# Performance work log

Measured on AMD Instinct MI355X. Metric: run time of the kernel, lower is better.

The kernel has to match this reference:

```python
import jax, jax.numpy as jnp
import numpy as np

D_MODEL, D_STATE, D_CONV, EXPAND = 1024, 16, 4, 2
D_INNER = EXPAND * D_MODEL           # 2048
DT_RANK = D_MODEL // 16              # 64
BATCH, SEQLEN = 2, 2048


def setup_inputs() -> dict:
    key = jax.random.key(0)
    ks = jax.random.split(key, 10)
    s = 0.02
    hidden_states = jax.random.normal(ks[0], (BATCH, SEQLEN, D_MODEL), jnp.float32)
    in_proj_w = jax.random.normal(ks[1], (2 * D_INNER, D_MODEL), jnp.float32) * s
    conv_w = jax.random.normal(ks[2], (D_INNER, 1, D_CONV), jnp.float32) * 0.3
    conv_b = jax.random.normal(ks[3], (D_INNER,), jnp.float32) * 0.1
    x_proj_w = jax.random.normal(ks[4], (DT_RANK + 2 * D_STATE, D_INNER), jnp.float32) * s
    dt_init_std = DT_RANK ** -0.5
    dt_proj_w = jax.random.uniform(ks[5], (D_INNER, DT_RANK), jnp.float32,
                                   minval=-dt_init_std, maxval=dt_init_std)
    # bias = inverse-softplus of dt sampled log-uniform in [1e-3, 1e-1]
    dt = jnp.exp(jax.random.uniform(ks[6], (D_INNER,), jnp.float32)
                 * (np.log(0.1) - np.log(0.001)) + np.log(0.001))
    dt = jnp.clip(dt, 1e-4, None)
    dt_proj_b = dt + jnp.log(-jnp.expm1(-dt))
    # A = repeat(arange(1, d_state+1), 'n -> d n')
    A_log = jnp.log(jnp.tile(jnp.arange(1, D_STATE + 1, dtype=jnp.float32), (D_INNER, 1)))
    Dp = jnp.ones((D_INNER,), jnp.float32)
    out_proj_w = jax.random.normal(ks[7], (D_MODEL, D_INNER), jnp.float32) * s
    return {
        'hidden_states': hidden_states, 'in_proj_w': in_proj_w,
        'conv_w': conv_w, 'conv_b': conv_b, 'x_proj_w': x_proj_w,
        'dt_proj_w': dt_proj_w, 'dt_proj_b': dt_proj_b,
        'A_log': A_log, 'D': Dp, 'out_proj_w': out_proj_w,
    }


def _mamba_fwd(hidden_states, in_proj_w, conv_w, conv_b, x_proj_w,
               dt_proj_w, dt_proj_b, A_log, D, out_proj_w):
    d_inner = in_proj_w.shape[0] // 2
    d_conv = conv_w.shape[-1]
    dt_rank = dt_proj_w.shape[1]
    d_state = A_log.shape[1]
    b = hidden_states.shape[0]

    # in_proj then split into x / z gate branches  -> [B, L, d_inner] each
    xz = hidden_states @ in_proj_w.T
    x, z = jnp.split(xz, 2, axis=-1)

    # depthwise causal conv1d + SiLU (pad left d_conv-1 == padding=d_conv-1 then trim)
    xc = x.transpose(0, 2, 1)                       # [B, d_inner, L]
    xc = jax.lax.conv_general_dilated(
        xc, conv_w, window_strides=(1,), padding=[(d_conv - 1, 0)],
        dimension_numbers=('NCH', 'OIH', 'NCH'), feature_group_count=d_inner)
    xl = jax.nn.silu(xc + conv_b[None, :, None]).transpose(0, 2, 1)  # [B, L, d_inner]

    # x_proj -> dt, B, C
    x_dbl = xl @ x_proj_w.T                         # [B, L, dt_rank + 2*d_state]
    dt, Bm, Cm = jnp.split(x_dbl, [dt_rank, dt_rank + d_state], axis=-1)
    delta = jax.nn.softplus(dt @ dt_proj_w.T + dt_proj_b)  # [B, L, d_inner]

    A = -jnp.exp(A_log)                             # [d_inner, d_state]

    def step(h, inputs):
        u_t, d_t, b_t, c_t = inputs  # [B,d_inner], [B,d_inner], [B,d_state], [B,d_state]
        dA = jnp.exp(d_t[..., None] * A)                      # [B, d_inner, d_state]
        h = dA * h + (d_t * u_t)[..., None] * b_t[:, None, :]
        y_t = jnp.einsum('bdn,bn->bd', h, c_t)
        return h, y_t

    h0 = jnp.zeros((b, d_inner, d_state), hidden_states.dtype)
    xs = (xl.transpose(1, 0, 2), delta.transpose(1, 0, 2),
          Bm.transpose(1, 0, 2), Cm.transpose(1, 0, 2))
    _, ys = jax.lax.scan(step, h0, xs)              # ys: [L, B, d_inner]
    y = ys.transpose(1, 0, 2)

    y = y + xl * D                                  # skip (D) term
    y = y * jax.nn.silu(z)                          # gate
    return y @ out_proj_w.T                         # [B, L, d_model]


def reference(hidden_states, in_proj_w, conv_w, conv_b, x_proj_w,
              dt_proj_w, dt_proj_b, A_log, D, out_proj_w):
    return _mamba_fwd(hidden_states, in_proj_w, conv_w, conv_b, x_proj_w,
                      dt_proj_w, dt_proj_b, A_log, D, out_proj_w)
```

## Files before the change

kernel.cpp:

```cpp
#include <hip/hip_runtime.h>

#define D_MODEL 1024
#define D_STATE 16
#define D_CONV  4
#define D_INNER 2048
#define DT_RANK 64
#define BATCH   2
#define SEQLEN  2048
#define NTOK    (BATCH * SEQLEN)
#define NCH     64
#define LC      (SEQLEN / NCH)
#define XKS     8
#define XNC     96


__device__ __forceinline__ float bf2f(unsigned short v) {
    union { unsigned int u; float f; } c; c.u = ((unsigned int)v) << 16; return c.f;
}
__device__ __forceinline__ unsigned short f2bf(float f) {
    union { unsigned int u; float f; } c; c.f = f;
    unsigned int r = c.u + 0x7FFF + ((c.u >> 16) & 1);
    return (unsigned short)(r >> 16);
}

__device__ __forceinline__ int sniff_bf(const void* Dp) {
    return (((const unsigned int*)Dp)[0] == 0x3F803F80u) ? 1 : 0;
}

__device__ __forceinline__ float ldF(const void* p, size_t idx, int isbf) {
    return isbf ? bf2f(((const unsigned short*)p)[idx]) : ((const float*)p)[idx];
}
__device__ __forceinline__ void ld16f(const float* p, float* o) {
#pragma unroll
    for (int q = 0; q < 4; q++) {
        float4 v = *(const float4*)(p + 4 * q);
        o[4 * q + 0] = v.x; o[4 * q + 1] = v.y; o[4 * q + 2] = v.z; o[4 * q + 3] = v.w;
    }
}

#define CVT_N0 (NTOK * D_MODEL)
#define CVT_N1 (2 * D_INNER * D_MODEL)
#define CVT_N2 (D_MODEL * D_INNER)
#define CVT_N3 (D_INNER * DT_RANK)
#define CVT_TOT (CVT_N0 + CVT_N1 + CVT_N2 + CVT_N3)

__device__ __forceinline__ void cvt8(const void* in, unsigned short* out,
                                     size_t e0, int isbf)
{
    if (isbf) {
        *(uint4*)(out + e0) = *(const uint4*)((const unsigned short*)in + e0);
    } else {
        const float* f = (const float*)in + e0;
        float4 a = *(const float4*)f;
        float4 b = *(const float4*)(f + 4);
        ushort4 o0 = { f2bf(a.x), f2bf(a.y), f2bf(a.z), f2bf(a.w) };
        ushort4 o1 = { f2bf(b.x), f2bf(b.y), f2bf(b.z), f2bf(b.w) };
        *(ushort4*)(out + e0)     = o0;
        *(ushort4*)(out + e0 + 4) = o1;
    }
}

__launch_bounds__(256)
__global__ void cvt_all(const void* __restrict__ hid, const void* __restrict__ ipw,
                        const void* __restrict__ opw, const void* __restrict__ dtw,
                        unsigned short* __restrict__ hidB, unsigned short* __restrict__ ipwB,
                        unsigned short* __restrict__ opwB, unsigned short* __restrict__ dtwB,
                        const void* __restrict__ Dp)
{
    const int isbf = sniff_bf(Dp);
    size_t e = ((size_t)blockIdx.x * 256 + threadIdx.x) * 8;
    if (e < CVT_N0) { cvt8(hid, hidB, e, isbf); return; }
    e -= CVT_N0;
    if (e < CVT_N1) { cvt8(ipw, ipwB, e, isbf); return; }
    e -= CVT_N1;
    if (e < CVT_N2) { cvt8(opw, opwB, e, isbf); return; }
    e -= CVT_N2;
    if (e < CVT_N3) { cvt8(dtw, dtwB, e, isbf); }
}

typedef __attribute__((ext_vector_type(8))) __bf16 bf16x8;
typedef __attribute__((ext_vector_type(4))) float  f32x4;

__global__ void mfma_probe(int* __restrict__ dmap) {
    __shared__ alignas(16) unsigned short As[16 * 32];
    __shared__ alignas(16) unsigned short Bs[16 * 32];
    const int t = threadIdx.x;
    const int q = t >> 4, l15 = t & 15;

    for (int idx = t; idx < 512; idx += 64) {
        As[idx] = f2bf((float)(idx >> 5));
        Bs[idx] = f2bf(0.03125f);
    }
    __syncthreads();
    bf16x8 a1 = *(const bf16x8*)&As[l15 * 32 + q * 8];
    bf16x8 b1 = *(const bf16x8*)&Bs[l15 * 32 + q * 8];
    f32x4 acc1 = {0.f, 0.f, 0.f, 0.f};
    acc1 = __builtin_amdgcn_mfma_f32_16x16x32_bf16(a1, b1, acc1, 0, 0, 0);
    __syncthreads();

    for (int idx = t; idx < 512; idx += 64) {
        As[idx] = f2bf(0.03125f);
        Bs[idx] = f2bf((float)(idx >> 5));
    }
    __syncthreads();
    bf16x8 a2 = *(const bf16x8*)&As[l15 * 32 + q * 8];
    bf16x8 b2 = *(const bf16x8*)&Bs[l15 * 32 + q * 8];
    f32x4 acc2 = {0.f, 0.f, 0.f, 0.f};
    acc2 = __builtin_amdgcn_mfma_f32_16x16x32_bf16(a2, b2, acc2, 0, 0, 0);

#pragma unroll
    for (int r = 0; r < 4; r++) {
        int ma = (int)(acc1[r] + 0.5f);
        int nb = (int)(acc2[r] + 0.5f);
        if (ma < 0 || ma > 15 || nb < 0 || nb > 15) { ma = q * 4 + r; nb = l15; }
        dmap[t * 4 + r] = ma | (nb << 4);
    }
}

__device__ __forceinline__ void gl2lds16(const void* g, void* l) {
    __builtin_amdgcn_global_load_lds(
        (const __attribute__((address_space(1))) unsigned int*)g,
        (__attribute__((address_space(3))) unsigned int*)l,
        16, 0, 0);
}

__device__ __forceinline__ void stage_half(const unsigned short* __restrict__ G,
                                           int grow0, int K, int k0,
                                           unsigned short* ldsAB, int half, int t)
{
    const int r8  = t >> 3;
    const int c8  = t & 7;
    const int swz = (c8 ^ (r8 & 7)) << 3;
#pragma unroll
    for (int j = 0; j < 2; j++) {
        const int row = half * 128 + j * 64 + r8;
        gl2lds16(&G[(size_t)(grow0 + row) * K + k0 + swz],
                 &ldsAB[row * 64 + c8 * 8]);
    }
}

__device__ __forceinline__ bf16x8 ldsfrag(const unsigned short* p, int row, int slot) {
    return *(const bf16x8*)&p[row * 64 + ((slot ^ (row & 7)) << 3)];
}

__launch_bounds__(512)
__global__ void gemm1_8ph(const unsigned short* __restrict__ A,
                          const unsigned short* __restrict__ B,
                          float* __restrict__ C,
                          int M, int N, int K,
                          const int* __restrict__ dmap)
{
    extern __shared__ __align__(16) unsigned short lds[];
    unsigned short* A0l = lds;
    unsigned short* B0l = lds + 16384;
    unsigned short* A1l = lds + 32768;
    unsigned short* B1l = lds + 49152;

    const int t    = threadIdx.x;
    const int lane = t & 63;
    const int w    = t >> 6;
    const int wm   = (w >> 2) * 128, wn = (w & 3) * 64;
    const int q    = lane >> 4, l15 = lane & 15;

    const int nbn  = N >> 8;
    const int nwg  = (M >> 8) * nbn;
    const int orig = blockIdx.x;
    const int wg   = (orig & 7) * (nwg >> 3) + (orig >> 3);
    const int bm   = wg / nbn, bn = wg % nbn;
    const int m0   = bm << 8, n0 = bn << 8;
    const int NT   = K >> 6;

    int mp[4];
#pragma unroll
    for (int r = 0; r < 4; r++) mp[r] = dmap[lane * 4 + r];

    f32x4 acc[8][4];
#pragma unroll
    for (int i = 0; i < 8; i++)
#pragma unroll
        for (int j = 0; j < 4; j++) acc[i][j] = (f32x4){0.f, 0.f, 0.f, 0.f};

    stage_half(B, n0, K, 0, B0l, 0, t);
    stage_half(B, n0, K, 0, B0l, 1, t);
    stage_half(A, m0, K, 0, A0l, 0, t);
    stage_half(A, m0, K, 0, A0l, 1, t);
    {
        const int k1 = (NT > 1 ? 64 : 0);
        stage_half(B, n0, K, k1, B1l, 0, t);
        stage_half(B, n0, K, k1, B1l, 1, t);
    }
    asm volatile("s_waitcnt vmcnt(4)" ::: "memory");
    __builtin_amdgcn_s_barrier();

#pragma unroll 2
    for (int tt = 0; tt < NT; ++tt) {
        const int p = tt & 1;
        const unsigned short* Ac = p ? A1l : A0l;
        const unsigned short* Bc = p ? B1l : B0l;
        unsigned short* Anx = p ? A0l : A1l;
        unsigned short* Bnx = p ? B1l : B0l;
        const int kA = (tt + 1 < NT ? tt + 1 : 0) << 6;
        const int kB = (tt + 2 < NT ? tt + 2 : 0) << 6;

        bf16x8 af[4][2], b0r[2][2], b1r[2][2];

#pragma unroll
        for (int i = 0; i < 4; i++)
#pragma unroll
            for (int ks = 0; ks < 2; ks++)
                af[i][ks] = ldsfrag(Ac, wm + i * 16 + l15, ks * 4 + q);
#pragma unroll
        for (int j = 0; j < 2; j++)
#pragma unroll
            for (int ks = 0; ks < 2; ks++)
                b0r[j][ks] = ldsfrag(Bc, wn + j * 16 + l15, ks * 4 + q);
        stage_half(A, m0, K, kA, Anx, 0, t);
        asm volatile("" ::: "memory");
        __builtin_amdgcn_s_barrier();
        __builtin_amdgcn_s_setprio(1);
#pragma unroll
        for (int i = 0; i < 4; i++)
#pragma unroll
            for (int j = 0; j < 2; j++)
#pragma unroll
                for (int ks = 0; ks < 2; ks++)
                    acc[i][j] = __builtin_amdgcn_mfma_f32_16x16x32_bf16(
                        af[i][ks], b0r[j][ks], acc[i][j], 0, 0, 0);
        __builtin_amdgcn_s_setprio(0);
        asm volatile("" ::: "memory");
        __builtin_amdgcn_s_barrier();

#pragma unroll
        for (int j = 0; j < 2; j++)
#pragma unroll
            for (int ks = 0; ks < 2; ks++)
                b1r[j][ks] = ldsfrag(Bc, wn + 32 + j * 16 + l15, ks * 4 + q);
        stage_half(A, m0, K, kA, Anx, 1, t);
        asm volatile("" ::: "memory");
        __builtin_amdgcn_s_barrier();
        __builtin_amdgcn_s_setprio(1);
#pragma unroll
        for (int i = 0; i < 4; i++)
#pragma unroll
            for (int j = 0; j < 2; j++)
#pragma unroll
                for (int ks = 0; ks < 2; ks++)
                    acc[i][2 + j] = __builtin_amdgcn_mfma_f32_16x16x32_bf16(
                        af[i][ks], b1r[j][ks], acc[i][2 + j], 0, 0, 0);
        __builtin_amdgcn_s_setprio(0);
        asm volatile("" ::: "memory");
        __builtin_amdgcn_s_barrier();

#pragma unroll
        for (int i = 0; i < 4; i++)
#pragma unroll
            for (int ks = 0; ks < 2; ks++)
                af[i][ks] = ldsfrag(Ac, wm + 64 + i * 16 + l15, ks * 4 + q);
        stage_half(B, n0, K, kB, Bnx, 0, t);
        asm volatile("" ::: "memory");
        __builtin_amdgcn_s_barrier();
        __builtin_amdgcn_s_setprio(1);
#pragma unroll
        for (int i = 0; i < 4; i++)
#pragma unroll
            for (int j = 0; j < 2; j++)
#pragma unroll
                for (int ks = 0; ks < 2; ks++)
                    acc[4 + i][2 + j] = __builtin_amdgcn_mfma_f32_16x16x32_bf16(
                        af[i][ks], b1r[j][ks], acc[4 + i][2 + j], 0, 0, 0);
        __builtin_amdgcn_s_setprio(0);
        asm volatile("" ::: "memory");
        __builtin_amdgcn_s_barrier();

        stage_half(B, n0, K, kB, Bnx, 1, t);
        asm volatile("" ::: "memory");
        __builtin_amdgcn_s_barrier();
        __builtin_amdgcn_s_setprio(1);
#pragma unroll
        for (int i = 0; i < 4; i++)
#pragma unroll
            for (int j = 0; j < 2; j++)
#pragma unroll
                for (int ks = 0; ks < 2; ks++)
                    acc[4 + i][j] = __builtin_amdgcn_mfma_f32_16x16x32_bf16(
                        af[i][ks], b0r[j][ks], acc[4 + i][j], 0, 0, 0);
        __builtin_amdgcn_s_setprio(0);
        asm volatile("s_waitcnt vmcnt(4)" ::: "memory");
        __builtin_amdgcn_s_barrier();
    }

#pragma unroll
    for (int i = 0; i < 8; i++) {
#pragma unroll
        for (int r = 0; r < 4; r++) {
            const int mo = mp[r] & 15, no = mp[r] >> 4;
            const int m = m0 + wm + i * 16 + mo;
#pragma unroll
            for (int j = 0; j < 4; j++) {
                const int n = n0 + wn + j * 16 + no;
                C[(size_t)m * N + n] = acc[i][j][r];
            }
        }
    }
}

__device__ __forceinline__ void stage_op(const unsigned short* __restrict__ A,
                                         const unsigned short* __restrict__ B,
                                         int m0, int n0, int K, int k0,
                                         unsigned short* Al, unsigned short* Bl, int t)
{
    const int r   = t >> 3;
    const int c8  = t & 7;
    const int swz = (c8 ^ (r & 7)) << 3;
#pragma unroll
    for (int j = 0; j < 4; j++) {
        const int row = j * 32 + r;
        gl2lds16(&A[(size_t)(m0 + row) * K + k0 + swz], &Al[row * 64 + c8 * 8]);
    }
#pragma unroll
    for (int j = 0; j < 2; j++) {
        const int row = j * 32 + r;
        gl2lds16(&B[(size_t)(n0 + row) * K + k0 + swz], &Bl[row * 64 + c8 * 8]);
    }
}

__launch_bounds__(256)
__global__ void gemm_op_2ph(const unsigned short* __restrict__ A,
                            const unsigned short* __restrict__ B,
                            float* __restrict__ C,
                            const int* __restrict__ dmap)
{
    constexpr int M = NTOK, N = D_MODEL, K = D_INNER;
    constexpr int NT = K / 64;
    __shared__ alignas(16) unsigned short Al[2][128 * 64];
    __shared__ alignas(16) unsigned short Bl[2][64 * 64];

    const int t    = threadIdx.x;
    const int lane = t & 63;
    const int w    = t >> 6;
    const int wm   = (w >> 1) * 64, wn = (w & 1) * 32;
    const int q    = lane >> 4, l15 = lane & 15;

    const int nbn  = N / 64;
    const int nwg  = (M / 128) * nbn;
    const int orig = blockIdx.x;
    const int wg   = (orig & 7) * (nwg >> 3) + (orig >> 3);
    const int bm   = wg / nbn, bn = wg % nbn;
    const int m0   = bm * 128, n0 = bn * 64;

    int mp[4];
#pragma unroll
    for (int r = 0; r < 4; r++) mp[r] = dmap[lane * 4 + r];

    f32x4 acc[4][2];
#pragma unroll
    for (int i = 0; i < 4; i++)
#pragma unroll
        for (int j = 0; j < 2; j++) acc[i][j] = (f32x4){0.f, 0.f, 0.f, 0.f};

    stage_op(A, B, m0, n0, K, 0, Al[0], Bl[0], t);
    asm volatile("s_waitcnt vmcnt(0)" ::: "memory");
    __builtin_amdgcn_s_barrier();

#pragma unroll 2
    for (int tt = 0; tt < NT - 1; ++tt) {
        const int cur = tt & 1;
        stage_op(A, B, m0, n0, K, (tt + 1) * 64, Al[cur ^ 1], Bl[cur ^ 1], t);

        bf16x8 af[4][2], bfr[2][2];
#pragma unroll
        for (int i = 0; i < 4; i++)
#pragma unroll
            for (int ks = 0; ks < 2; ks++)
                af[i][ks] = ldsfrag(Al[cur], wm + i * 16 + l15, ks * 4 + q);
#pragma unroll
        for (int j = 0; j < 2; j++)
#pragma unroll
            for (int ks = 0; ks < 2; ks++)
                bfr[j][ks] = ldsfrag(Bl[cur], wn + j * 16 + l15, ks * 4 + q);
        __builtin_amdgcn_s_setprio(1);
#pragma unroll
        for (int i = 0; i < 4; i++)
#pragma unroll
            for (int j = 0; j < 2; j++)
#pragma unroll
                for (int ks = 0; ks < 2; ks++)
                    acc[i][j] = __builtin_amdgcn_mfma_f32_16x16x32_bf16(
                        af[i][ks], bfr[j][ks], acc[i][j], 0, 0, 0);
        __builtin_amdgcn_s_setprio(0);
        asm volatile("s_waitcnt vmcnt(0)" ::: "memory");
        __builtin_amdgcn_s_barrier();
    }

    {
        const int cur = (NT - 1) & 1;
        bf16x8 af[4][2], bfr[2][2];
#pragma unroll
        for (int i = 0; i < 4; i++)
#pragma unroll
            for (int ks = 0; ks < 2; ks++)
                af[i][ks] = ldsfrag(Al[cur], wm + i * 16 + l15, ks * 4 + q);
#pragma unroll
        for (int j = 0; j < 2; j++)
#pragma unroll
            for (int ks = 0; ks < 2; ks++)
                bfr[j][ks] = ldsfrag(Bl[cur], wn + j * 16 + l15, ks * 4 + q);
#pragma unroll
        for (int i = 0; i < 4; i++)
#pragma unroll
            for (int j = 0; j < 2; j++)
#pragma unroll
                for (int ks = 0; ks < 2; ks++)
                    acc[i][j] = __builtin_amdgcn_mfma_f32_16x16x32_bf16(
                        af[i][ks], bfr[j][ks], acc[i][j], 0, 0, 0);
    }

#pragma unroll
    for (int i = 0; i < 4; i++) {
#pragma unroll
        for (int r = 0; r < 4; r++) {
            const int mo = mp[r] & 15, no = mp[r] >> 4;
            const int m = m0 + wm + i * 16 + mo;
#pragma unroll
            for (int j = 0; j < 2; j++) {
                const int n = n0 + wn + j * 16 + no;
                C[(size_t)m * N + n] = acc[i][j][r];
            }
        }
    }
}

__launch_bounds__(256)
__global__ void gemm_dt(const unsigned short* __restrict__ A,
                        const unsigned short* __restrict__ B,
                        float* __restrict__ C,
                        const int* __restrict__ dmap,
                        const void* __restrict__ bias,
                        const void* __restrict__ Dp)
{
    constexpr int M = NTOK, N = D_INNER, K = DT_RANK;
    __shared__ alignas(16) unsigned short Al[128 * 64];
    __shared__ alignas(16) unsigned short Bl[128 * 64];

    const int t    = threadIdx.x;
    const int lane = t & 63;
    const int w    = t >> 6;
    const int wm   = (w >> 1) * 64, wn = (w & 1) * 64;
    const int q    = lane >> 4, l15 = lane & 15;

    const int nbn  = N / 128;
    const int nwg  = (M / 128) * nbn;
    const int orig = blockIdx.x;
    const int wg   = (orig & 7) * (nwg >> 3) + (orig >> 3);
    const int bm   = wg / nbn, bn = wg % nbn;
    const int m0   = bm * 128, n0 = bn * 128;

    int mp[4];
#pragma unroll
    for (int r = 0; r < 4; r++) mp[r] = dmap[lane * 4 + r];

    {
        const int r   = t >> 3;
        const int c8  = t & 7;
        const int swz = (c8 ^ (r & 7)) << 3;
#pragma unroll
        for (int j = 0; j < 4; j++) {
            const int row = j * 32 + r;
            gl2lds16(&A[(size_t)(m0 + row) * K + swz], &Al[row * 64 + c8 * 8]);
            gl2lds16(&B[(size_t)(n0 + row) * K + swz], &Bl[row * 64 + c8 * 8]);
        }
    }
    asm volatile("s_waitcnt vmcnt(0)" ::: "memory");
    __builtin_amdgcn_s_barrier();

    f32x4 acc[4][4];
#pragma unroll
    for (int i = 0; i < 4; i++)
#pragma unroll
        for (int j = 0; j < 4; j++) acc[i][j] = (f32x4){0.f, 0.f, 0.f, 0.f};

    bf16x8 af[4][2], bfr[4][2];
#pragma unroll
    for (int i = 0; i < 4; i++)
#pragma unroll
        for (int ks = 0; ks < 2; ks++)
            af[i][ks] = ldsfrag(Al, wm + i * 16 + l15, ks * 4 + q);
#pragma unroll
    for (int j = 0; j < 4; j++)
#pragma unroll
        for (int ks = 0; ks < 2; ks++)
            bfr[j][ks] = ldsfrag(Bl, wn + j * 16 + l15, ks * 4 + q);
#pragma unroll
    for (int i = 0; i < 4; i++)
#pragma unroll
        for (int j = 0; j < 4; j++)
#pragma unroll
            for (int ks = 0; ks < 2; ks++)
                acc[i][j] = __builtin_amdgcn_mfma_f32_16x16x32_bf16(
                    af[i][ks], bfr[j][ks], acc[i][j], 0, 0, 0);

    const int isbf = sniff_bf(Dp);
#pragma unroll
    for (int i = 0; i < 4; i++) {
#pragma unroll
        for (int r = 0; r < 4; r++) {
            const int mo = mp[r] & 15, no = mp[r] >> 4;
            const int m = m0 + wm + i * 16 + mo;
#pragma unroll
            for (int j = 0; j < 4; j++) {
                const int n = n0 + wn + j * 16 + no;
                float v = acc[i][j][r] + ldF(bias, n, isbf);
                v = fmaxf(v, 0.f) + __logf(1.f + __expf(-fabsf(v)));
                C[(size_t)m * N + n] = v;
            }
        }
    }
}

__launch_bounds__(256)
__global__ void xproj_splitk(const float* __restrict__ A,
                             const float* __restrict__ B,
                             float* __restrict__ part)
{
    __shared__ alignas(16) float As[16][68];
    __shared__ alignas(16) float Bs[16][68];
    const int t  = threadIdx.x;
    const int m0 = blockIdx.y * 64, n0 = blockIdx.x * 64;
    const int koff = blockIdx.z * (D_INNER / XKS);
    const int lr = t >> 2;
    const int lk = (t & 3) * 4;
    const int tm = t >> 4, tn = t & 15;

    float acc[4][4];
#pragma unroll
    for (int i = 0; i < 4; i++)
#pragma unroll
        for (int j = 0; j < 4; j++) acc[i][j] = 0.f;

    for (int k0 = koff; k0 < koff + D_INNER / XKS; k0 += 16) {
        float av[4], bv[4];
        {
            const int m = m0 + lr;
            float4 p = *(const float4*)&A[(size_t)m * D_INNER + k0 + lk];
            av[0] = p.x; av[1] = p.y; av[2] = p.z; av[3] = p.w;
        }
        {
            const int n = n0 + lr;
            if (n < XNC) {
                float4 p = *(const float4*)&B[(size_t)n * D_INNER + k0 + lk];
                bv[0] = p.x; bv[1] = p.y; bv[2] = p.z; bv[3] = p.w;
            } else { bv[0] = bv[1] = bv[2] = bv[3] = 0.f; }
        }
        __syncthreads();
#pragma unroll
        for (int i = 0; i < 4; i++) { As[lk + i][lr] = av[i]; Bs[lk + i][lr] = bv[i]; }
        __syncthreads();

#pragma unroll
        for (int kk = 0; kk < 16; kk++) {
            float4 a = *(const float4*)&As[kk][tm * 4];
            float4 b = *(const float4*)&Bs[kk][tn * 4];
            float aa[4] = { a.x, a.y, a.z, a.w };
            float bb[4] = { b.x, b.y, b.z, b.w };
#pragma unroll
            for (int i = 0; i < 4; i++)
#pragma unroll
                for (int j = 0; j < 4; j++) acc[i][j] = fmaf(aa[i], bb[j], acc[i][j]);
        }
    }

    float* out = part + (size_t)blockIdx.z * NTOK * XNC;
#pragma unroll
    for (int i = 0; i < 4; i++) {
        const int m = m0 + tm * 4 + i;
#pragma unroll
        for (int j = 0; j < 4; j++) {
            const int n = n0 + tn * 4 + j;
            if (n < XNC) out[(size_t)m * XNC + n] = acc[i][j];
        }
    }
}

__launch_bounds__(256)
__global__ void xproj_reduce(const float* __restrict__ part, float* __restrict__ xdbl,
                             unsigned short* __restrict__ xdt)
{
    const int idx = blockIdx.x * 256 + threadIdx.x;
    float s = 0.f;
#pragma unroll
    for (int z = 0; z < XKS; z++) s += part[(size_t)z * NTOK * XNC + idx];
    xdbl[idx] = s;
    const int m = idx / XNC;
    const int col = idx - m * XNC;
    if (col < 64) xdt[m * 64 + col] = f2bf(s);
}

__launch_bounds__(256)
__global__ void conv_silu(const float* __restrict__ xz,
                          const void* __restrict__ conv_w,
                          const void* __restrict__ conv_b,
                          float* __restrict__ xl,
                          const void* __restrict__ Dp)
{
    const int isbf = sniff_bf(Dp);
    const int gid = blockIdx.x * 256 + threadIdx.x;
    const int dq  = gid & (D_INNER / 4 - 1);
    const int tg  = gid >> 9;
    const int d0  = dq * 4;
    const int tok0 = tg * 4;
    const int l0  = tok0 & (SEQLEN - 1);

    float w[4][4], bias[4];
#pragma unroll
    for (int dd = 0; dd < 4; dd++) {
        bias[dd] = ldF(conv_b, d0 + dd, isbf);
#pragma unroll
        for (int j = 0; j < 4; j++) w[dd][j] = ldF(conv_w, (d0 + dd) * 4 + j, isbf);
    }

    float4 x[7];
    const float* rowp = xz + (size_t)tok0 * (2 * D_INNER) + d0;
#pragma unroll
    for (int k = 0; k < 7; k++) {
        const int off = k - 3;
        if (l0 + off >= 0)
            x[k] = *(const float4*)(rowp + (ptrdiff_t)off * (2 * D_INNER));
        else
            x[k] = (float4){0.f, 0.f, 0.f, 0.f};
    }

#pragma unroll
    for (int tn = 0; tn < 4; tn++) {
        float a0 = bias[0], a1 = bias[1], a2 = bias[2], a3 = bias[3];
#pragma unroll
        for (int j = 0; j < 4; j++) {
            const float4 v = x[tn + j];
            a0 = fmaf(v.x, w[0][j], a0);
            a1 = fmaf(v.y, w[1][j], a1);
            a2 = fmaf(v.z, w[2][j], a2);
            a3 = fmaf(v.w, w[3][j], a3);
        }
        float4 o;
        o.x = a0 / (1.f + __expf(-a0));
        o.y = a1 / (1.f + __expf(-a1));
        o.z = a2 / (1.f + __expf(-a2));
        o.w = a3 / (1.f + __expf(-a3));
        *(float4*)&xl[(size_t)(tok0 + tn) * D_INNER + d0] = o;
    }
}

__device__ __forceinline__ void mk_dA(float dv, const float An[16], int pw, float* dA)
{
    if (pw) {
        const float E = __expf(dv * An[0]);
        dA[0] = E;
        const float E2 = E * E;          dA[1] = E2;
        const float E4 = E2 * E2;        dA[3] = E4;
        const float E8 = E4 * E4;        dA[7] = E8;
        dA[2]  = E2 * E;
        dA[4]  = E4 * E;   dA[5]  = E4 * E2;  dA[6]  = dA[5] * E;
        dA[8]  = E8 * E;   dA[9]  = E8 * E2;  dA[10] = dA[9] * E;
        dA[11] = E8 * E4;  dA[12] = dA[11] * E;
        dA[13] = dA[11] * E2; dA[14] = dA[13] * E; dA[15] = E8 * E8;
    } else {
#pragma unroll
        for (int n = 0; n < 16; n++) dA[n] = __expf(dv * An[n]);
    }
}

__device__ __forceinline__ int chk_pw(const float An[16])
{
    int pw = 1;
#pragma unroll
    for (int n = 1; n < 16; n++)
        pw = pw && (fabsf(An[n] - (float)(n + 1) * An[0]) <= 3e-4f * (float)(n + 1));
    return pw;
}

__device__ __forceinline__ void scan_step(float h[16], float dv, float uv,
                                          const float Bv[16], const float An[16], int pw)
{
    float dA[16]; mk_dA(dv, An, pw, dA);
    const float du = dv * uv;
#pragma unroll
    for (int n = 0; n < 16; n++) h[n] = fmaf(dA[n], h[n], du * Bv[n]);
}

__device__ __forceinline__ float scan_step_y(float h[16], float dv, float uv,
                                             const float Bv[16], const float Cv[16],
                                             const float An[16], int pw, float Dd)
{
    float dA[16]; mk_dA(dv, An, pw, dA);
    const float du = dv * uv;
    float s[16];
#pragma unroll
    for (int n = 0; n < 16; n++) {
        h[n] = fmaf(dA[n], h[n], du * Bv[n]);
        s[n] = h[n] * Cv[n];
    }
#pragma unroll
    for (int n = 0; n < 8; n++) s[n] += s[n + 8];
#pragma unroll
    for (int n = 0; n < 4; n++) s[n] += s[n + 4];
    s[0] += s[2]; s[1] += s[3];
    return s[0] + s[1] + uv * Dd;
}

__launch_bounds__(256)
__global__ void scan_chunk(const float* __restrict__ dlt,
                           const float* __restrict__ xl,
                           const float* __restrict__ xdbl,
                           const void* __restrict__ A_log,
                           float* __restrict__ S,
                           float* __restrict__ sumD,
                           const void* __restrict__ Dp)
{
    const int isbf = sniff_bf(Dp);
    const int t  = threadIdx.x;
    const int dg = blockIdx.x & 7;
    const int c  = (blockIdx.x >> 3) & (NCH - 1);
    const int b  = blockIdx.x >> 9;
    const int d  = dg * 256 + t;

    float An[16], h[16];
#pragma unroll
    for (int n = 0; n < 16; n++) {
        An[n] = -expf(ldF(A_log, d * 16 + n, isbf));
        h[n] = 0.f;
    }
    const int pw = chk_pw(An);
    float sd = 0.f;
    const size_t r0 = (size_t)b * SEQLEN + c * LC;

    float dv0 = dlt[r0 * D_INNER + d];
    float uv0 = xl [r0 * D_INNER + d];
    float Bv0[16]; ld16f(&xdbl[r0 * 96 + 64], Bv0);

    for (int i = 0; i < LC; i += 2) {
        const size_t r1 = r0 + i + 1;
        float dv1 = dlt[r1 * D_INNER + d];
        float uv1 = xl [r1 * D_INNER + d];
        float Bv1[16]; ld16f(&xdbl[r1 * 96 + 64], Bv1);

        scan_step(h, dv0, uv0, Bv0, An, pw);
        sd += dv0;

        const size_t r2 = r0 + ((i + 2 < LC) ? (i + 2) : (i + 1));
        dv0 = dlt[r2 * D_INNER + d];
        uv0 = xl [r2 * D_INNER + d];
        ld16f(&xdbl[r2 * 96 + 64], Bv0);

        scan_step(h, dv1, uv1, Bv1, An, pw);
        sd += dv1;
    }

    const size_t base = (((size_t)b * NCH + c) * 16) * D_INNER + d;
#pragma unroll
    for (int n = 0; n < 16; n++) S[base + (size_t)n * D_INNER] = h[n];
    sumD[((size_t)b * NCH + c) * D_INNER + d] = sd;
}

__launch_bounds__(256)
__global__ void scan_combine(float* __restrict__ S,
                             const float* __restrict__ sumD,
                             const void* __restrict__ A_log,
                             const void* __restrict__ Dp)
{
    const int isbf = sniff_bf(Dp);
    const int g = blockIdx.x * 256 + threadIdx.x;
    const int d = g & (D_INNER - 1);
    const int n = (g >> 11) & 15;
    const int b = g >> 15;
    const float An = -expf(ldF(A_log, d * 16 + n, isbf));

    float hs = 0.f;
    float Sc = S[(((size_t)b * NCH + 0) * 16 + n) * D_INNER + d];
    float sd = sumD[((size_t)b * NCH + 0) * D_INNER + d];
    for (int c = 0; c < NCH; c++) {
        const int cn = (c + 1 < NCH) ? c + 1 : c;
        const float Scn = S[(((size_t)b * NCH + cn) * 16 + n) * D_INNER + d];
        const float sdn = sumD[((size_t)b * NCH + cn) * D_INNER + d];
        S[(((size_t)b * NCH + c) * 16 + n) * D_INNER + d] = hs;
        hs = fmaf(__expf(An * sd), hs, Sc);
        Sc = Scn; sd = sdn;
    }
}

__launch_bounds__(256)
__global__ void scan_apply(const float* __restrict__ dlt,
                           const float* __restrict__ xl,
                           const float* __restrict__ xdbl,
                           const float* __restrict__ xz,
                           const void* __restrict__ A_log,
                           const void* __restrict__ Dp,
                           const float* __restrict__ S,
                           unsigned short* __restrict__ yg)
{
    const int isbf = sniff_bf(Dp);
    const int t  = threadIdx.x;
    const int dg = blockIdx.x & 7;
    const int c  = (blockIdx.x >> 3) & (NCH - 1);
    const int b  = blockIdx.x >> 9;
    const int d  = dg * 256 + t;

    float An[16], h[16];
    const size_t base = (((size_t)b * NCH + c) * 16) * D_INNER + d;
#pragma unroll
    for (int n = 0; n < 16; n++) {
        An[n] = -expf(ldF(A_log, d * 16 + n, isbf));
        h[n] = S[base + (size_t)n * D_INNER];
    }
    const int pw = chk_pw(An);
    const float Dd = ldF(Dp, d, isbf);
    const size_t r0 = (size_t)b * SEQLEN + c * LC;

    float dv0 = dlt[r0 * D_INNER + d];
    float uv0 = xl [r0 * D_INNER + d];
    float zv0 = xz [r0 * (2 * D_INNER) + D_INNER + d];
    float Bv0[16], Cv0[16];
    ld16f(&xdbl[r0 * 96 + 64], Bv0);
    ld16f(&xdbl[r0 * 96 + 80], Cv0);

    for (int i = 0; i < LC; i += 2) {
        const size_t ra = r0 + i + 1;
        float dv1 = dlt[ra * D_INNER + d];
        float uv1 = xl [ra * D_INNER + d];
        float zv1 = xz [ra * (2 * D_INNER) + D_INNER + d];
        float Bv1[16], Cv1[16];
        ld16f(&xdbl[ra * 96 + 64], Bv1);
        ld16f(&xdbl[ra * 96 + 80], Cv1);

        {
            const float yv = scan_step_y(h, dv0, uv0, Bv0, Cv0, An, pw, Dd);
            yg[(r0 + i) * D_INNER + d] = f2bf(yv * (zv0 / (1.f + __expf(-zv0))));
        }

        const size_t rb = r0 + ((i + 2 < LC) ? (i + 2) : (i + 1));
        dv0 = dlt[rb * D_INNER + d];
        uv0 = xl [rb * D_INNER + d];
        zv0 = xz [rb * (2 * D_INNER) + D_INNER + d];
        ld16f(&xdbl[rb * 96 + 64], Bv0);
        ld16f(&xdbl[rb * 96 + 80], Cv0);

        {
            const float yv = scan_step_y(h, dv1, uv1, Bv1, Cv1, An, pw, Dd);
            yg[ra * D_INNER + d] = f2bf(yv * (zv1 / (1.f + __expf(-zv1))));
        }
    }
}

extern "C" void kernel_launch(void* const* d_in, const int* in_sizes, int n_in,
                              void* d_out, int out_size, void* d_ws, size_t ws_size,
                              hipStream_t stream)
{
    const void* hidden     = d_in[0];
    const void* in_proj_w  = d_in[1];
    const void* conv_w     = d_in[2];
    const void* conv_b     = d_in[3];
    const void* x_proj_w   = d_in[4];
    const void* dt_proj_w  = d_in[5];
    const void* dt_proj_b  = d_in[6];
    const void* A_log      = d_in[7];
    const void* Dp         = d_in[8];
    const void* out_proj_w = d_in[9];

    char* ws = (char*)d_ws;
    float*          xz   = (float*)(ws);
    float*          xl   = (float*)(ws + 67108864ull);
    float*          xdbl = (float*)(ws + 100663296ull);
    float*          dlt  = (float*)(ws + 102236160ull);
    unsigned short* yg   = (unsigned short*)(ws + 135790592ull);
    unsigned short* opwB = (unsigned short*)(ws + 152567808ull);
    unsigned short* xdt  = (unsigned short*)(ws + 156762112ull);
    unsigned short* dtwB = (unsigned short*)(ws + 157286400ull);
    float*          S    = (float*)(ws + 169345280ull);
    float*          sumD = (float*)(ws + 186122496ull);
    int*            dmap = (int*)  (ws + 187171072ull);
    unsigned short* hidB  = (unsigned short*)(ws + 102236160ull);
    unsigned short* ipwB  = (unsigned short*)(ws + 102236160ull + 8388608ull);
    float*          xpart = (float*)(ws + 102236160ull);

    dim3 blk(256);

    mfma_probe<<<dim3(1), dim3(64), 0, stream>>>(dmap);

    cvt_all<<<dim3(CVT_TOT / (256 * 8)), blk, 0, stream>>>(
        hidden, in_proj_w, out_proj_w, dt_proj_w, hidB, ipwB, opwB, dtwB, Dp);

    hipFuncSetAttribute((const void*)gemm1_8ph,
                        hipFuncAttributeMaxDynamicSharedMemorySize, 131072);
    gemm1_8ph<<<dim3((NTOK / 256) * (2 * D_INNER / 256)), dim3(512), 131072, stream>>>(
        hidB, ipwB, xz, NTOK, 2 * D_INNER, D_MODEL, dmap);

    conv_silu<<<dim3((NTOK / 4) * (D_INNER / 4) / 256), blk, 0, stream>>>(
        xz, conv_w, conv_b, xl, Dp);

    xproj_splitk<<<dim3(2, 64, XKS), blk, 0, stream>>>(
        xl, (const float*)x_proj_w, xpart);
    xproj_reduce<<<dim3(NTOK * XNC / 256), blk, 0, stream>>>(xpart, xdbl, xdt);

    gemm_dt<<<dim3((NTOK / 128) * (D_INNER / 128)), blk, 0, stream>>>(
        xdt, dtwB, dlt, dmap, dt_proj_b, Dp);

    scan_chunk<<<dim3(BATCH * NCH * (D_INNER / 256)), blk, 0, stream>>>(
        dlt, xl, xdbl, A_log, S, sumD, Dp);
    scan_combine<<<dim3(BATCH * 16 * D_INNER / 256), blk, 0, stream>>>(
        S, sumD, A_log, Dp);
    scan_apply<<<dim3(BATCH * NCH * (D_INNER / 256)), blk, 0, stream>>>(
        dlt, xl, xdbl, xz, A_log, Dp, S, yg);

    gemm_op_2ph<<<dim3((NTOK / 128) * (D_MODEL / 64)), blk, 0, stream>>>(
        yg, opwB, (float*)d_out, dmap);
}
```

Baseline: 316.8 us.

## Split scan state across two half-waves and fold MFMA probe into convert kernel

The chunked scan kernels now give each channel two lanes, each holding 8 of the 16 state elements. The per-step y reduction is finished with a cross-lane shuffle, and the grids double in size. This cuts registers per thread and raises parallelism and occupancy, at the cost of duplicated per-channel loads (delta, u, z) and half the lanes idling on the y store. Separately, the one-block MFMA layout probe is merged into block 0 of the conversion kernel to save a launch.

```diff
diff --git a/kernel.cpp b/kernel.cpp
--- a/kernel.cpp
+++ b/kernel.cpp
@@ -30,11 +30,54 @@
 __device__ __forceinline__ float ldF(const void* p, size_t idx, int isbf) {
     return isbf ? bf2f(((const unsigned short*)p)[idx]) : ((const float*)p)[idx];
 }
-__device__ __forceinline__ void ld16f(const float* p, float* o) {
-#pragma unroll
-    for (int q = 0; q < 4; q++) {
+__device__ __forceinline__ void ld8f(const float* p, float* o) {
+#pragma unroll
+    for (int q = 0; q < 2; q++) {
         float4 v = *(const float4*)(p + 4 * q);
         o[4 * q + 0] = v.x; o[4 * q + 1] = v.y; o[4 * q + 2] = v.z; o[4 * q + 3] = v.w;
+    }
+}
+
+typedef __attribute__((ext_vector_type(8))) __bf16 bf16x8;
+typedef __attribute__((ext_vector_type(4))) float  f32x4;
+
+__device__ void probe_dmap_block(int t, int* __restrict__ dmap)
+{
+    __shared__ alignas(16) unsigned short PAs[16 * 32];
+    __shared__ alignas(16) unsigned short PBs[16 * 32];
+    const int q = (t & 63) >> 4, l15 = t & 15;
+
+    if (t < 64)
+        for (int idx = t; idx < 512; idx += 64) {
+            PAs[idx] = f2bf((float)(idx >> 5));
+            PBs[idx] = f2bf(0.03125f);
+        }
+    __syncthreads();
+    f32x4 acc1 = {0.f, 0.f, 0.f, 0.f};
+    if (t < 64) {
+        bf16x8 a1 = *(const bf16x8*)&PAs[l15 * 32 + q * 8];
+        bf16x8 b1 = *(const bf16x8*)&PBs[l15 * 32 + q * 8];
+        acc1 = __builtin_amdgcn_mfma_f32_16x16x32_bf16(a1, b1, acc1, 0, 0, 0);
+    }
+    __syncthreads();
+    if (t < 64)
+        for (int idx = t; idx < 512; idx += 64) {
+            PAs[idx] = f2bf(0.03125f);
+            PBs[idx] = f2bf((float)(idx >> 5));
+        }
+    __syncthreads();
+    if (t < 64) {
+        bf16x8 a2 = *(const bf16x8*)&PAs[l15 * 32 + q * 8];
+        bf16x8 b2 = *(const bf16x8*)&PBs[l15 * 32 + q * 8];
+        f32x4 acc2 = {0.f, 0.f, 0.f, 0.f};
+        acc2 = __builtin_amdgcn_mfma_f32_16x16x32_bf16(a2, b2, acc2, 0, 0, 0);
+#pragma unroll
+        for (int r = 0; r < 4; r++) {
+            int ma = (int)(acc1[r] + 0.5f);
+            int nb = (int)(acc2[r] + 0.5f);
+            if (ma < 0 || ma > 15 || nb < 0 || nb > 15) { ma = q * 4 + r; nb = l15; }
+            dmap[t * 4 + r] = ma | (nb << 4);
+        }
     }
 }
 
@@ -65,8 +108,10 @@
                         const void* __restrict__ opw, const void* __restrict__ dtw,
                         unsigned short* __restrict__ hidB, unsigned short* __restrict__ ipwB,
                         unsigned short* __restrict__ opwB, unsigned short* __restrict__ dtwB,
-                        const void* __restrict__ Dp)
-{
+                        const void* __restrict__ Dp, int* __restrict__ dmap)
+{
+    if (blockIdx.x == 0) probe_dmap_block(threadIdx.x, dmap);
+
     const int isbf = sniff_bf(Dp);
     size_t e = ((size_t)blockIdx.x * 256 + threadIdx.x) * 8;
     if (e < CVT_N0) { cvt8(hid, hidB, e, isbf); return; }
@@ -78,45 +123,6 @@
     if (e < CVT_N3) { cvt8(dtw, dtwB, e, isbf); }
 }
 
-typedef __attribute__((ext_vector_type(8))) __bf16 bf16x8;
-typedef __attribute__((ext_vector_type(4))) float  f32x4;
-
-__global__ void mfma_probe(int* __restrict__ dmap) {
-    __shared__ alignas(16) unsigned short As[16 * 32];
-    __shared__ alignas(16) unsigned short Bs[16 * 32];
-    const int t = threadIdx.x;
-    const int q = t >> 4, l15 = t & 15;
-
-    for (int idx = t; idx < 512; idx += 64) {
-        As[idx] = f2bf((float)(idx >> 5));
-        Bs[idx] = f2bf(0.03125f);
-    }
-    __syncthreads();
-    bf16x8 a1 = *(const bf16x8*)&As[l15 * 32 + q * 8];
-    bf16x8 b1 = *(const bf16x8*)&Bs[l15 * 32 + q * 8];
-    f32x4 acc1 = {0.f, 0.f, 0.f, 0.f};
-    acc1 = __builtin_amdgcn_mfma_f32_16x16x32_bf16(a1, b1, acc1, 0, 0, 0);
-    __syncthreads();
-
-    for (int idx = t; idx < 512; idx += 64) {
-        As[idx] = f2bf(0.03125f);
-        Bs[idx] = f2bf((float)(idx >> 5));
-    }
-    __syncthreads();
-    bf16x8 a2 = *(const bf16x8*)&As[l15 * 32 + q * 8];
-    bf16x8 b2 = *(const bf16x8*)&Bs[l15 * 32 + q * 8];
-    f32x4 acc2 = {0.f, 0.f, 0.f, 0.f};
-    acc2 = __builtin_amdgcn_mfma_f32_16x16x32_bf16(a2, b2, acc2, 0, 0, 0);
-
-#pragma unroll
-    for (int r = 0; r < 4; r++) {
-        int ma = (int)(acc1[r] + 0.5f);
-        int nb = (int)(acc2[r] + 0.5f);
-        if (ma < 0 || ma > 15 || nb < 0 || nb > 15) { ma = q * 4 + r; nb = l15; }
-        dmap[t * 4 + r] = ma | (nb << 4);
-    }
-}
-
 __device__ __forceinline__ void gl2lds16(const void* g, void* l) {
     __builtin_amdgcn_global_load_lds(
         (const __attribute__((address_space(1))) unsigned int*)g,
@@ -649,61 +655,56 @@
     }
 }
 
-__device__ __forceinline__ void mk_dA(float dv, const float An[16], int pw, float* dA)
+__device__ __forceinline__ void mk_dA8(float dv, const float An[8], float An0,
+                                       int nh, int pw, float* dA)
 {
     if (pw) {
-        const float E = __expf(dv * An[0]);
-        dA[0] = E;
-        const float E2 = E * E;          dA[1] = E2;
-        const float E4 = E2 * E2;        dA[3] = E4;
-        const float E8 = E4 * E4;        dA[7] = E8;
-        dA[2]  = E2 * E;
-        dA[4]  = E4 * E;   dA[5]  = E4 * E2;  dA[6]  = dA[5] * E;
-        dA[8]  = E8 * E;   dA[9]  = E8 * E2;  dA[10] = dA[9] * E;
-        dA[11] = E8 * E4;  dA[12] = dA[11] * E;
-        dA[13] = dA[11] * E2; dA[14] = dA[13] * E; dA[15] = E8 * E8;
+        const float E  = __expf(dv * An0);
+        const float E2 = E * E;
+        const float E4 = E2 * E2;
+        const float E8 = E4 * E4;
+        if (nh == 0) {
+            dA[0] = E;        dA[1] = E2;       dA[2] = E2 * E;   dA[3] = E4;
+            dA[4] = E4 * E;   dA[5] = E4 * E2;  dA[6] = dA[5] * E; dA[7] = E8;
+        } else {
+            dA[0] = E8 * E;   dA[1] = E8 * E2;  dA[2] = dA[1] * E; dA[3] = E8 * E4;
+            dA[4] = dA[3] * E; dA[5] = dA[3] * E2; dA[6] = dA[5] * E; dA[7] = E8 * E8;
+        }
     } else {
 #pragma unroll
-        for (int n = 0; n < 16; n++) dA[n] = __expf(dv * An[n]);
-    }
-}
-
-__device__ __forceinline__ int chk_pw(const float An[16])
-{
-    int pw = 1;
-#pragma unroll
-    for (int n = 1; n < 16; n++)
-        pw = pw && (fabsf(An[n] - (float)(n + 1) * An[0]) <= 3e-4f * (float)(n + 1));
-    return pw;
-}
-
-__device__ __forceinline__ void scan_step(float h[16], float dv, float uv,
-                                          const float Bv[16], const float An[16], int pw)
-{
-    float dA[16]; mk_dA(dv, An, pw, dA);
+        for (int n = 0; n < 8; n++) dA[n] = __expf(dv * An[n]);
+    }
+}
+
+__device__ __forceinline__ void scan_step8(float h[8], float dv, float uv,
+                                           const float Bv[8], const float An[8],
+                                           float An0, int nh, int pw)
+{
+    float dA[8]; mk_dA8(dv, An, An0, nh, pw, dA);
     const float du = dv * uv;
 #pragma unroll
-    for (int n = 0; n < 16; n++) h[n] = fmaf(dA[n], h[n], du * Bv[n]);
-}
-
-__device__ __forceinline__ float scan_step_y(float h[16], float dv, float uv,
-                                             const float Bv[16], const float Cv[16],
-                                             const float An[16], int pw, float Dd)
-{
-    float dA[16]; mk_dA(dv, An, pw, dA);
+    for (int n = 0; n < 8; n++) h[n] = fmaf(dA[n], h[n], du * Bv[n]);
+}
+
+__device__ __forceinline__ float scan_step_y8(float h[8], float dv, float uv,
+                                              const float Bv[8], const float Cv[8],
+                                              const float An[8], float An0,
+                                              int nh, int pw, float Dd)
+{
+    float dA[8]; mk_dA8(dv, An, An0, nh, pw, dA);
     const float du = dv * uv;
-    float s[16];
-#pragma unroll
-    for (int n = 0; n < 16; n++) {
+    float s[8];
+#pragma unroll
+    for (int n = 0; n < 8; n++) {
         h[n] = fmaf(dA[n], h[n], du * Bv[n]);
         s[n] = h[n] * Cv[n];
     }
 #pragma unroll
-    for (int n = 0; n < 8; n++) s[n] += s[n + 8];
-#pragma unroll
     for (int n = 0; n < 4; n++) s[n] += s[n + 4];
     s[0] += s[2]; s[1] += s[3];
-    return s[0] + s[1] + uv * Dd;
+    float r = s[0] + s[1];
+    r += __shfl_xor(r, 32);
+    return r + uv * Dd;
 }
 
 __launch_bounds__(256)
@@ -716,48 +717,58 @@
                            const void* __restrict__ Dp)
 {
     const int isbf = sniff_bf(Dp);
-    const int t  = threadIdx.x;
-    const int dg = blockIdx.x & 7;
-    const int c  = (blockIdx.x >> 3) & (NCH - 1);
-    const int b  = blockIdx.x >> 9;
-    const int d  = dg * 256 + t;
-
-    float An[16], h[16];
-#pragma unroll
-    for (int n = 0; n < 16; n++) {
-        An[n] = -expf(ldF(A_log, d * 16 + n, isbf));
+    const int t    = threadIdx.x;
+    const int lane = t & 63;
+    const int wv   = t >> 6;
+    const int dg   = blockIdx.x & 15;
+    const int c    = (blockIdx.x >> 4) & (NCH - 1);
+    const int b    = blockIdx.x >> 10;
+    const int d    = dg * 128 + wv * 32 + (lane & 31);
+    const int nh   = lane >> 5;
+    const int n0   = nh * 8;
+
+    const float An0 = -expf(ldF(A_log, (size_t)d * 16, isbf));
+    float An[8], h[8];
+#pragma unroll
+    for (int n = 0; n < 8; n++) {
+        An[n] = -expf(ldF(A_log, (size_t)d * 16 + n0 + n, isbf));
         h[n] = 0.f;
     }
-    const int pw = chk_pw(An);
+    int pw = 1;
+#pragma unroll
+    for (int n = 0; n < 8; n++)
+        pw = pw && (fabsf(An[n] - (float)(n0 + n + 1) * An0)
+                    <= 3e-4f * (float)(n0 + n + 1));
+
     float sd = 0.f;
     const size_t r0 = (size_t)b * SEQLEN + c * LC;
 
     float dv0 = dlt[r0 * D_INNER + d];
     float uv0 = xl [r0 * D_INNER + d];
-    float Bv0[16]; ld16f(&xdbl[r0 * 96 + 64], Bv0);
+    float Bv0[8]; ld8f(&xdbl[r0 * 96 + 64 + n0], Bv0);
 
     for (int i = 0; i < LC; i += 2) {
         const size_t r1 = r0 + i + 1;
         float dv1 = dlt[r1 * D_INNER + d];
         float uv1 = xl [r1 * D_INNER + d];
-        float Bv1[16]; ld16f(&xdbl[r1 * 96 + 64], Bv1);
-
-        scan_step(h, dv0, uv0, Bv0, An, pw);
+        float Bv1[8]; ld8f(&xdbl[r1 * 96 + 64 + n0], Bv1);
+
+        scan_step8(h, dv0, uv0, Bv0, An, An0, nh, pw);
         sd += dv0;
 
         const size_t r2 = r0 + ((i + 2 < LC) ? (i + 2) : (i + 1));
         dv0 = dlt[r2 * D_INNER + d];
         uv0 = xl [r2 * D_INNER + d];
-        ld16f(&xdbl[r2 * 96 + 64], Bv0);
-
-        scan_step(h, dv1, uv1, Bv1, An, pw);
+        ld8f(&xdbl[r2 * 96 + 64 + n0], Bv0);
+
+        scan_step8(h, dv1, uv1, Bv1, An, An0, nh, pw);
         sd += dv1;
     }
 
-    const size_t base = (((size_t)b * NCH + c) * 16) * D_INNER + d;
-#pragma unroll
-    for (int n = 0; n < 16; n++) S[base + (size_t)n * D_INNER] = h[n];
-    sumD[((size_t)b * NCH + c) * D_INNER + d] = sd;
+    const size_t base2 = (((size_t)b * NCH + c) * 16 + n0) * D_INNER + d;
+#pragma unroll
+    for (int n = 0; n < 8; n++) S[base2 + (size_t)n * D_INNER] = h[n];
+    if (nh == 0) sumD[((size_t)b * NCH + c) * D_INNER + d] = sd;
 }
 
 __launch_bounds__(256)
@@ -797,54 +808,66 @@
                            unsigned short* __restrict__ yg)
 {
     const int isbf = sniff_bf(Dp);
-    const int t  = threadIdx.x;
-    const int dg = blockIdx.x & 7;
-    const int c  = (blockIdx.x >> 3) & (NCH - 1);
-    const int b  = blockIdx.x >> 9;
-    const int d  = dg * 256 + t;
-
-    float An[16], h[16];
-    const size_t base = (((size_t)b * NCH + c) * 16) * D_INNER + d;
-#pragma unroll
-    for (int n = 0; n < 16; n++) {
-        An[n] = -expf(ldF(A_log, d * 16 + n, isbf));
-        h[n] = S[base + (size_t)n * D_INNER];
-    }
-    const int pw = chk_pw(An);
+    const int t    = threadIdx.x;
+    const int lane = t & 63;
+    const int wv   = t >> 6;
+    const int dg   = blockIdx.x & 15;
+    const int c    = (blockIdx.x >> 4) & (NCH - 1);
+    const int b    = blockIdx.x >> 10;
+    const int d    = dg * 128 + wv * 32 + (lane & 31);
+    const int nh   = lane >> 5;
+    const int n0   = nh * 8;
+
+    const float An0 = -expf(ldF(A_log, (size_t)d * 16, isbf));
+    float An[8], h[8];
+    const size_t base2 = (((size_t)b * NCH + c) * 16 + n0) * D_INNER + d;
+#pragma unroll
+    for (int n = 0; n < 8; n++) {
+        An[n] = -expf(ldF(A_log, (size_t)d * 16 + n0 + n, isbf));
+        h[n] = S[base2 + (size_t)n * D_INNER];
+    }
+    int pw = 1;
+#pragma unroll
+    for (int n = 0; n < 8; n++)
+        pw = pw && (fabsf(An[n] - (float)(n0 + n + 1) * An0)
+                    <= 3e-4f * (float)(n0 + n + 1));
+
     const float Dd = ldF(Dp, d, isbf);
     const size_t r0 = (size_t)b * SEQLEN + c * LC;
 
     float dv0 = dlt[r0 * D_INNER + d];
     float uv0 = xl [r0 * D_INNER + d];
     float zv0 = xz [r0 * (2 * D_INNER) + D_INNER + d];
-    float Bv0[16], Cv0[16];
-    ld16f(&xdbl[r0 * 96 + 64], Bv0);
-    ld16f(&xdbl[r0 * 96 + 80], Cv0);
+    float Bv0[8], Cv0[8];
+    ld8f(&xdbl[r0 * 96 + 64 + n0], Bv0);
+    ld8f(&xdbl[r0 * 96 + 80 + n0], Cv0);
 
     for (int i = 0; i < LC; i += 2) {
         const size_t ra = r0 + i + 1;
         float dv1 = dlt[ra * D_INNER + d];
         float uv1 = xl [ra * D_INNER + d];
         float zv1 = xz [ra * (2 * D_INNER) + D_INNER + d];
-        float Bv1[16], Cv1[16];
-        ld16f(&xdbl[ra * 96 + 64], Bv1);
-        ld16f(&xdbl[ra * 96 + 80], Cv1);
+        float Bv1[8], Cv1[8];
+        ld8f(&xdbl[ra * 96 + 64 + n0], Bv1);
+        ld8f(&xdbl[ra * 96 + 80 + n0], Cv1);
 
         {
-            const float yv = scan_step_y(h, dv0, uv0, Bv0, Cv0, An, pw, Dd);
-            yg[(r0 + i) * D_INNER + d] = f2bf(yv * (zv0 / (1.f + __expf(-zv0))));
+            const float yv = scan_step_y8(h, dv0, uv0, Bv0, Cv0, An, An0, nh, pw, Dd);
+            if (nh == 0)
+                yg[(r0 + i) * D_INNER + d] = f2bf(yv * (zv0 / (1.f + __expf(-zv0))));
         }
 
         const size_t rb = r0 + ((i + 2 < LC) ? (i + 2) : (i + 1));
         dv0 = dlt[rb * D_INNER + d];
         uv0 = xl [rb * D_INNER + d];
         zv0 = xz [rb * (2 * D_INNER) + D_INNER + d];
-        ld16f(&xdbl[rb * 96 + 64], Bv0);
-        ld16f(&xdbl[rb * 96 + 80], Cv0);
+        ld8f(&xdbl[rb * 96 + 64 + n0], Bv0);
+        ld8f(&xdbl[rb * 96 + 80 + n0], Cv0);
 
         {
-            const float yv = scan_step_y(h, dv1, uv1, Bv1, Cv1, An, pw, Dd);
-            yg[ra * D_INNER + d] = f2bf(yv * (zv1 / (1.f + __expf(-zv1))));
+            const float yv = scan_step_y8(h, dv1, uv1, Bv1, Cv1, An, An0, nh, pw, Dd);
+            if (nh == 0)
+                yg[ra * D_INNER + d] = f2bf(yv * (zv1 / (1.f + __expf(-zv1))));
         }
     }
 }
@@ -882,10 +905,8 @@
 
     dim3 blk(256);
 
-    mfma_probe<<<dim3(1), dim3(64), 0, stream>>>(dmap);
-
     cvt_all<<<dim3(CVT_TOT / (256 * 8)), blk, 0, stream>>>(
-        hidden, in_proj_w, out_proj_w, dt_proj_w, hidB, ipwB, opwB, dtwB, Dp);
+        hidden, in_proj_w, out_proj_w, dt_proj_w, hidB, ipwB, opwB, dtwB, Dp, dmap);
 
     hipFuncSetAttribute((const void*)gemm1_8ph,
                         hipFuncAttributeMaxDynamicSharedMemorySize, 131072);
@@ -902,11 +923,11 @@
     gemm_dt<<<dim3((NTOK / 128) * (D_INNER / 128)), blk, 0, stream>>>(
         xdt, dtwB, dlt, dmap, dt_proj_b, Dp);
 
-    scan_chunk<<<dim3(BATCH * NCH * (D_INNER / 256)), blk, 0, stream>>>(
+    scan_chunk<<<dim3(BATCH * NCH * (D_INNER / 128)), blk, 0, stream>>>(
         dlt, xl, xdbl, A_log, S, sumD, Dp);
     scan_combine<<<dim3(BATCH * 16 * D_INNER / 256), blk, 0, stream>>>(
         S, sumD, A_log, Dp);
-    scan_apply<<<dim3(BATCH * NCH * (D_INNER / 256)), blk, 0, stream>>>(
+    scan_apply<<<dim3(BATCH * NCH * (D_INNER / 128)), blk, 0, stream>>>(
         dlt, xl, xdbl, xz, A_log, Dp, S, yg);
 
     gemm_op_2ph<<<dim3((NTOK / 128) * (D_MODEL / 64)), blk, 0, stream>>>(
```

Measured after the change: 336.8 us. +6.3%, slower.
